# Kernel optimization log

Hardware: AMD Instinct MI355X
Metric: run time of the kernel (lower is better)

The kernel has to match this reference:

```python
import jax, jax.numpy as jnp
import numpy as np
from jax.scipy.special import logsumexp

B, L = 32, 128
NEG = -1e9
SPAN_LAMB = 0.5


def setup_inputs() -> dict:
    key = jax.random.key(0)
    ks = jax.random.split(key, 8)
    span_logits = jax.random.normal(ks[0], (B, L, L, 2), jnp.float32)
    ph = jax.random.normal(ks[1], (B, L, L), jnp.float32)
    pt = jax.random.normal(ks[2], (B, L, L), jnp.float32)
    ph_arc = jax.random.normal(ks[3], (B, L, L), jnp.float32)
    spans_ind = jax.random.randint(ks[4], (B, L, L), 0, 3, jnp.int32)
    ph_ind = jax.random.randint(ks[5], (B, L, L), 0, 2, jnp.int32)
    pt_ind = jax.random.randint(ks[6], (B, L, L), 0, 2, jnp.int32)
    lens = jax.random.randint(ks[7], (B,), L // 2, L + 1, jnp.int32)
    i = jnp.arange(L)
    # maskspan[b,i,j] = valid right-closed span i..j within sentence b; row 0 sums to lens
    maskspan = (i[None, :, None] <= i[None, None, :]) & (i[None, None, :] < lens[:, None, None])
    maskarc = (i[None, :, None] < lens[:, None, None]) & (i[None, None, :] < lens[:, None, None])
    return dict(span_logits=span_logits, ph=ph, pt=pt, ph_arc=ph_arc,
                spans_ind=spans_ind, ph_ind=ph_ind, pt_ind=pt_ind,
                maskspan=maskspan, maskarc=maskarc)


def _inside_logZ(span_logits, lens):
    # CYK inside algorithm over right-closed spans; returns sum_b logZ_b.
    scores = logsumexp(span_logits, axis=-1)  # [B,L,L] span score = lse over labels
    Ln = scores.shape[1]
    ar = jnp.arange(Ln)
    # width-0 base: s[i,i] = scores[i,i]
    s0 = jnp.where(jnp.eye(Ln, dtype=bool)[None], scores, NEG)
    li = ar[:, None] + ar[None, :]        # [L,L]: left child right end i+k
    ri = li + 1                           # right child left end i+k+1
    li_c = jnp.clip(li, 0, Ln - 1)
    ri_c = jnp.clip(ri, 0, Ln - 1)

    def step(s, w):
        j = ar + w
        jc = jnp.clip(j, 0, Ln - 1)
        left = s[:, ar[:, None], li_c]                 # [B,L,L] left[b,i,k]=s[b,i,i+k]
        right = s[:, ri_c, jc[:, None]]                # right[b,i,k]=s[b,i+k+1,i+w]
        comb = jnp.where(ar[None, None, :] < w, left + right, NEG)
        new = scores[:, ar, jc] + logsumexp(comb, axis=-1)  # [B,L]
        valid = (j < Ln)[None, :]
        cur = s[:, ar, jc]
        s = s.at[:, ar, jc].set(jnp.where(valid, new, cur))
        return s, None

    s, _ = jax.lax.scan(step, s0, jnp.arange(1, Ln))
    logZ = jnp.take_along_axis(s[:, 0, :], (lens - 1)[:, None], axis=1)[:, 0]
    return logZ.sum()


def _bce_mean(x, y, m):
    # stable BCEWithLogits, mean over masked elements
    l = jnp.maximum(x, 0.0) - x * y + jnp.log1p(jnp.exp(-jnp.abs(x)))
    return jnp.where(m, l, 0.0).sum() / m.sum().astype(jnp.float32)


def reference(span_logits, ph, pt, ph_arc, spans_ind, ph_ind, pt_ind, maskspan, maskarc):
    lens = maskspan[:, 0].sum(-1)                         # [B]
    spans_b = jnp.where(spans_ind > 0, spans_ind - 1, spans_ind).astype(bool)
    # label marginals = d logZ / d span_logits (matches torch autograd-based cyk)
    marginals = jax.grad(_inside_logZ)(span_logits, lens)  # [B,L,L,2]
    pos_mask = maskspan & spans_b
    neg_mask = maskspan & (~spans_b)
    pos_loss = jnp.log(jnp.where(pos_mask, jnp.maximum(marginals[..., 1], 1e-38), 1.0)).sum()
    neg_loss = jnp.log(jnp.where(neg_mask, jnp.maximum(marginals[..., 0], 1e-38), 1.0)).sum()
    loss_spans = -(pos_loss + neg_loss) / lens.sum().astype(jnp.float32)
    loss_ph = _bce_mean(ph, ph_ind.astype(jnp.float32), maskarc)
    loss_pt = _bce_mean(pt, pt_ind.astype(jnp.float32), maskarc)
    return SPAN_LAMB * loss_spans + (1.0 - SPAN_LAMB) * (loss_ph + loss_pt)
```

## Files before the change

kernel.cpp:

```cpp
#include <hip/hip_runtime.h>
#include <hip/hip_bf16.h>
#include <float.h>

#define NB 32
#define NBCE 32
#define L 128
#define NT 1024
#define R 132
#define PAD 160
#define LOGMIN -87.49823f

__device__ __forceinline__ int mask_mode(const void* p) {
    unsigned int v = ((const unsigned int*)p)[0];
    if (v == 1u) return 1;
    if (v == 0x3F800000u) return 2;
    return 0;
}
__device__ __forceinline__ bool mask_at(const void* p, int mode, int idx) {
    if (mode == 1) return ((const int*)p)[idx] != 0;
    if (mode == 2) return ((const float*)p)[idx] != 0.0f;
    return ((const unsigned char*)p)[idx] != 0;
}

__device__ __forceinline__ float lse2(float a, float b) {
    return fmaxf(a, b) + log1pf(__expf(-fabsf(a - b)));
}

template<int C>
__device__ __forceinline__ float dppf(float x) {
    return __int_as_float(__builtin_amdgcn_mov_dpp(__float_as_int(x), C, 0xF, 0xF, true));
}
__device__ __forceinline__ float bfly8_max(float x) {
    x = fmaxf(x, dppf<0xB1>(x));
    x = fmaxf(x, dppf<0x4E>(x));
    x = fmaxf(x, dppf<0x141>(x));
    return x;
}
__device__ __forceinline__ float bfly8_add(float x) {
    x += dppf<0xB1>(x);
    x += dppf<0x4E>(x);
    x += dppf<0x141>(x);
    return x;
}

template<int NUMAX>
__device__ __forceinline__ void load_pairs(float* buf, int sub, int lo, int hi,
                                           const float* p1, const float* p2, float& mloc) {
    p1 += sub; p2 += sub;
#pragma unroll
    for (int kk = 0; kk < NUMAX; kk += 2) {
        if (kk * 8 >= hi) break;
        const int o0 = kk * 8, o1 = o0 + 8;
        float a0 = p1[o0] + p2[o0];
        float a1 = p1[o1] + p2[o1];
        const int t0 = sub + o0, t1 = sub + o1;
        a0 = (t0 >= lo && t0 < hi) ? a0 : -FLT_MAX;
        a1 = (t1 >= lo && t1 < hi) ? a1 : -FLT_MAX;
        buf[kk] = a0; buf[kk + 1] = a1;
        mloc = fmaxf(mloc, fmaxf(a0, a1));
    }
}
template<int NUMAX>
__device__ __forceinline__ void sum_exp8(const float* buf, int hi, float M, float& s) {
#pragma unroll
    for (int kk = 0; kk < NUMAX; kk += 2) {
        if (kk * 8 >= hi) break;
        s += __expf(buf[kk] - M) + __expf(buf[kk + 1] - M);
    }
}

__global__ __launch_bounds__(NT, 1) void tree_dp_kernel(
    const float* __restrict__ logits,
    const int*   __restrict__ spans_ind,
    const void*  __restrict__ maskspan,
    const float* __restrict__ ph, const float* __restrict__ pt,
    const int* __restrict__ ph_ind, const int* __restrict__ pt_ind,
    const void* __restrict__ maskarc,
    double*      __restrict__ ws)
{
    const int tid = threadIdx.x;

    if (blockIdx.x >= NB) {
        const int mode = mask_mode(maskarc);
        const int tot = NB * L * L;
        double sph = 0.0, spt = 0.0, cnt = 0.0;
        for (int idx = (blockIdx.x - NB) * NT + tid; idx < tot; idx += NBCE * NT) {
            if (mask_at(maskarc, mode, idx)) {
                float x = ph[idx]; float y = (float)ph_ind[idx];
                sph += (double)(fmaxf(x, 0.0f) - x * y + log1pf(__expf(-fabsf(x))));
                x = pt[idx]; y = (float)pt_ind[idx];
                spt += (double)(fmaxf(x, 0.0f) - x * y + log1pf(__expf(-fabsf(x))));
                cnt += 1.0;
            }
        }
        for (int off = 32; off > 0; off >>= 1) {
            sph += __shfl_down(sph, off);
            spt += __shfl_down(spt, off);
            cnt += __shfl_down(cnt, off);
        }
        if ((tid & 63) == 0) {
            atomicAdd(&ws[2], sph); atomicAdd(&ws[3], spt); atomicAdd(&ws[4], cnt);
        }
        return;
    }

    __shared__ float Am[L * R + PAD];
    __shared__ float Gm[L * R + PAD];

    const int b = blockIdx.x;
    const int mbase = b * L * L;
    const int mode = mask_mode(maskspan);

    int pred = (tid < L) && mask_at(maskspan, mode, mbase + tid);
    const int n = __syncthreads_count(pred);

    const float* lg = logits + (size_t)b * L * L * 2;
    const int* si = spans_ind + mbase;

    for (int e = tid; e < L * L; e += NT) {
        int ii = e >> 7, jj = e & (L - 1);
        if (ii <= jj && jj < n) {
            const float* p = lg + (size_t)e * 2;
            float v = lse2(p[0], p[1]);
            Am[ii * R + jj] = v; Am[jj * R + ii] = v;
            Gm[ii * R + jj] = v; Gm[jj * R + ii] = v;
        }
    }
    __syncthreads();

    const int i = tid >> 3;
    const int sub = tid & 7;
    double local = 0.0;
    float buf1[16], buf2[16];

    float ld0 = 0.f, pv = 0.f, scij = 0.f, rjd = 0.f;
    float m_part = -FLT_MAX, s_part = 0.f;
    if (i < n) ld0 = Am[i * R + i];
    if (i < n - 1) scij = Am[i * R + i + 1];

    for (int w = 1; w < n; ++w) {
        const int c = n - w;
        const int j = i + w;
        float r0 = 0.f;
        if (i < c) r0 = Am[j * R + i + 1];
        float nsc = 0.f, nrjd = 0.f, mloc = -FLT_MAX;
        const bool pf = (i < c - 1);
        if (pf) {
            nsc  = Am[i * R + (j + 1)];
            nrjd = Am[(j + 1) * R + (j + 1)];
            load_pairs<16>(buf1, sub, 1, w, &Am[i * R + i], &Am[(j + 1) * R + i + 1], mloc);
        }
        if (i < c) {
            float ta = ld0 + r0;
            float tb = (w >= 2) ? (pv + rjd) : -FLT_MAX;
            float M = fmaxf(fmaxf(m_part, ta), tb);
            float S = s_part * __expf(m_part - M) + __expf(ta - M) + __expf(tb - M);
            float val = scij + M + __logf(S);
            if (sub == 0) { Am[i * R + j] = val; Am[j * R + i] = val; }
            pv = val;
        }
        m_part = -FLT_MAX; s_part = 0.f;
        if (pf) {
            float Mp = bfly8_max(mloc);
            float s = 0.f;
            sum_exp8<16>(buf1, w, Mp, s);
            s_part = bfly8_add(s);
            m_part = Mp;
            scij = nsc; rjd = nrjd;
        }
        __syncthreads();
    }

    const float logZ = Am[n - 1];

    float adI = 0.f, adJ = 0.f, scO = 0.f;
    if (i >= 1 && i < n) adI = Am[(i - 1) * R + (i - 1)];
    if (i == 0) pv = Gm[n - 1];

    m_part = -FLT_MAX; s_part = 0.f;
    {
        const int w1 = n - 2;
        if (i < n - w1) {
            const int j1 = i + w1;
            scO = Gm[i * R + j1];
            if (j1 < n - 1) adJ = Am[(j1 + 1) * R + (j1 + 1)];
            const int nt1 = n - 1 - j1;
            float mloc = -FLT_MAX;
            load_pairs<16>(buf1, sub, 1, nt1, &Gm[i * R + j1 + 1], &Am[(j1 + 1) * R + j1 + 1], mloc);
            load_pairs<16>(buf2, sub, 0, i - 1, &Gm[j1 * R], &Am[(i - 1) * R], mloc);
            float Mp = bfly8_max(mloc);
            float s = 0.f;
            sum_exp8<16>(buf1, nt1, Mp, s);
            sum_exp8<16>(buf2, i - 1, Mp, s);
            s_part = bfly8_add(s);
            m_part = Mp;
        }
    }

    for (int w = n - 2; w >= 0; --w) {
        const int c = n - w;
        const int j = i + w;
        float r0g = 0.f;
        if (i < c && i >= 1) r0g = Gm[j * R + (i - 1)];
        float nsc = 0.f, nadJ = 0.f, mloc = -FLT_MAX;
        const bool pf = (w >= 1) && (i < c + 1);
        int nt1 = 0;
        if (pf) {
            const int j1 = i + w - 1;
            nsc = Gm[i * R + j1];
            if (j1 < n - 1) nadJ = Am[(j1 + 1) * R + (j1 + 1)];
            nt1 = n - 1 - j1;
            load_pairs<16>(buf1, sub, 1, nt1, &Gm[i * R + j1 + 1], &Am[(j1 + 1) * R + j1 + 1], mloc);
            load_pairs<16>(buf2, sub, 0, i - 1, &Gm[j1 * R], &Am[(i - 1) * R], mloc);
        }
        if (i < c) {
            float g1n = (j < n - 1) ? (pv + adJ) : -FLT_MAX;
            float g2n = (i >= 1) ? (r0g + adI) : -FLT_MAX;
            float M = fmaxf(fmaxf(m_part, g1n), g2n);
            float S = s_part * __expf(m_part - M) + __expf(g1n - M) + __expf(g2n - M);
            if (w >= 1) {
                float val = scO + M + __logf(S);
                if (sub == 0) { Gm[i * R + j] = val; Gm[j * R + i] = val; }
                pv = val;
            } else if (sub == 0) {
                float beta_ii = M + __logf(S);
                const float* p = lg + ((size_t)i * L + i) * 2;
                float lc = (si[i * L + i] == 2) ? p[1] : p[0];
                local += (double)fmaxf(beta_ii - logZ + lc, LOGMIN);
            }
        }
        m_part = -FLT_MAX; s_part = 0.f;
        if (pf) {
            float Mp = bfly8_max(mloc);
            float s = 0.f;
            sum_exp8<16>(buf1, nt1, Mp, s);
            sum_exp8<16>(buf2, i - 1, Mp, s);
            s_part = bfly8_add(s);
            m_part = Mp;
            scO = nsc; adJ = nadJ;
        }
        __syncthreads();
    }

    for (int e = tid; e < L * L; e += NT) {
        int ii = e >> 7, jj = e & (L - 1);
        if (ii < jj && jj < n) {
            const float* p = lg + (size_t)e * 2;
            float a = p[0], cc = p[1];
            float sc = lse2(a, cc);
            float lc = (si[e] == 2) ? cc : a;
            float logm = Am[ii * R + jj] + Gm[ii * R + jj] - logZ + lc - 2.0f * sc;
            local += (double)fmaxf(logm, LOGMIN);
        }
    }

    for (int off = 32; off > 0; off >>= 1)
        local += __shfl_down(local, off);
    if ((tid & 63) == 0) atomicAdd(&ws[0], local);
    if (tid == 0) atomicAdd(&ws[1], (double)n);
}

__global__ void finalize_kernel(const double* __restrict__ ws, float* __restrict__ out) {
    double loss_spans = -ws[0] / ws[1];
    double bce = (ws[2] + ws[3]) / ws[4];
    out[0] = (float)(0.5 * loss_spans + 0.5 * bce);
}

extern "C" void kernel_launch(void* const* d_in, const int* in_sizes, int n_in,
                              void* d_out, int out_size, void* d_ws, size_t ws_size,
                              hipStream_t stream) {
    (void)in_sizes; (void)n_in; (void)out_size; (void)ws_size;
    const float* span_logits = (const float*)d_in[0];
    const float* ph          = (const float*)d_in[1];
    const float* pt          = (const float*)d_in[2];
    const int*   spans_ind   = (const int*)d_in[4];
    const int*   ph_ind      = (const int*)d_in[5];
    const int*   pt_ind      = (const int*)d_in[6];
    const void*  maskspan    = d_in[7];
    const void*  maskarc     = d_in[8];
    double* ws = (double*)d_ws;
    float* out = (float*)d_out;

    hipMemsetAsync(d_ws, 0, 5 * sizeof(double), stream);
    hipLaunchKernelGGL(tree_dp_kernel, dim3(NB + NBCE), dim3(NT), 0, stream,
                       span_logits, spans_ind, maskspan,
                       ph, pt, ph_ind, pt_ind, maskarc, ws);
    hipLaunchKernelGGL(finalize_kernel, dim3(1), dim3(1), 0, stream, ws, out);
}
```

Baseline: 343.6 us.

## Pack inside/outside into one square matrix and run two sentences per block

Stores inside scores in the upper triangle and outside scores in the lower triangle of a single shared matrix, so each block holds two sentences and only 16 DP blocks are launched. Each 512-thread half processes one sentence, with every 8-lane group handling two cells per width. The register prefetch pipeline is dropped in favour of a simpler per-cell load, reduce and store. This halves the number of DP blocks and removes the separate outside matrix, but every thread now does two cells serially per step and both halves synchronise to the longer sentence.

```diff
diff --git a/kernel.cpp b/kernel.cpp
--- a/kernel.cpp
+++ b/kernel.cpp
@@ -1,13 +1,13 @@
 #include <hip/hip_runtime.h>
-#include <hip/hip_bf16.h>
 #include <float.h>
 
-#define NB 32
+#define NBATCH 32
+#define NBDP 16
 #define NBCE 32
 #define L 128
 #define NT 1024
 #define R 132
-#define PAD 160
+#define SQ_SIZE (L * R + 8)
 #define LOGMIN -87.49823f
 
 __device__ __forceinline__ int mask_mode(const void* p) {
@@ -30,13 +30,13 @@
 __device__ __forceinline__ float dppf(float x) {
     return __int_as_float(__builtin_amdgcn_mov_dpp(__float_as_int(x), C, 0xF, 0xF, true));
 }
-__device__ __forceinline__ float bfly8_max(float x) {
+__device__ __forceinline__ float bfly_max8(float x) {
     x = fmaxf(x, dppf<0xB1>(x));
     x = fmaxf(x, dppf<0x4E>(x));
     x = fmaxf(x, dppf<0x141>(x));
     return x;
 }
-__device__ __forceinline__ float bfly8_add(float x) {
+__device__ __forceinline__ float bfly_add8(float x) {
     x += dppf<0xB1>(x);
     x += dppf<0x4E>(x);
     x += dppf<0x141>(x);
@@ -44,29 +44,60 @@
 }
 
 template<int NUMAX>
-__device__ __forceinline__ void load_pairs(float* buf, int sub, int lo, int hi,
-                                           const float* p1, const float* p2, float& mloc) {
-    p1 += sub; p2 += sub;
+__device__ __forceinline__ void load_rc(float* v, int sub, int nterm,
+                                        const float* p1, const float* p2, float& mloc) {
+    p1 += sub; p2 += sub * R;
 #pragma unroll
-    for (int kk = 0; kk < NUMAX; kk += 2) {
-        if (kk * 8 >= hi) break;
-        const int o0 = kk * 8, o1 = o0 + 8;
-        float a0 = p1[o0] + p2[o0];
-        float a1 = p1[o1] + p2[o1];
-        const int t0 = sub + o0, t1 = sub + o1;
-        a0 = (t0 >= lo && t0 < hi) ? a0 : -FLT_MAX;
-        a1 = (t1 >= lo && t1 < hi) ? a1 : -FLT_MAX;
-        buf[kk] = a0; buf[kk + 1] = a1;
+    for (int m = 0; m < NUMAX; m += 2) {
+        if (m * 8 >= nterm) break;
+        const int o0 = m * 8, o1 = o0 + 8;
+        float a0 = p1[o0] + p2[o0 * R];
+        float a1 = p1[o1] + p2[o1 * R];
+        a0 = (sub + o0 < nterm) ? a0 : -FLT_MAX;
+        a1 = (sub + o1 < nterm) ? a1 : -FLT_MAX;
+        v[m] = a0; v[m + 1] = a1;
         mloc = fmaxf(mloc, fmaxf(a0, a1));
     }
 }
 template<int NUMAX>
-__device__ __forceinline__ void sum_exp8(const float* buf, int hi, float M, float& s) {
+__device__ __forceinline__ void sum_exp8(const float* v, int nterm, float M, float& s) {
 #pragma unroll
-    for (int kk = 0; kk < NUMAX; kk += 2) {
-        if (kk * 8 >= hi) break;
-        s += __expf(buf[kk] - M) + __expf(buf[kk + 1] - M);
-    }
+    for (int m = 0; m < NUMAX; m += 2) {
+        if (m * 8 >= nterm) break;
+        s += __expf(v[m] - M) + __expf(v[m + 1] - M);
+    }
+}
+
+template<int NU>
+__device__ __forceinline__ void inside_cell(float* SQm, int i, int w, int sub) {
+    const int j = i + w;
+    float v[NU]; float mloc = -FLT_MAX;
+    load_rc<NU>(v, sub, w, &SQm[i * R + i], &SQm[(i + 1) * R + j], mloc);
+    float M = bfly_max8(mloc);
+    float s = 0.0f;
+    sum_exp8<NU>(v, w, M, s);
+    float S = bfly_add8(s);
+    if (sub == 0) SQm[i * R + j] += M + __logf(S);
+}
+
+template<int NU, int NV>
+__device__ __forceinline__ float outside_cell(float* SQm, int i, int j, int n, int sub, bool store) {
+    float v1[NU], v2[NV]; float mloc = -FLT_MAX;
+    const int ntU = n - 1 - j;
+    load_rc<NU>(v1, sub, ntU, &SQm[(j + 1) * R + (j + 1)], &SQm[(j + 1) * R + i], mloc);
+    const float* p2v = &SQm[(i >= 1 ? i - 1 : 0)];
+    load_rc<NV>(v2, sub, i, &SQm[j * R], p2v, mloc);
+    float M = bfly_max8(mloc);
+    float s = 0.0f;
+    sum_exp8<NU>(v1, ntU, M, s);
+    sum_exp8<NV>(v2, i, M, s);
+    float S = bfly_add8(s);
+    float out = 0.0f;
+    if (sub == 0) {
+        out = M + __logf(S);
+        if (store) SQm[j * R + i] += out;
+    }
+    return out;
 }
 
 __global__ __launch_bounds__(NT, 1) void tree_dp_kernel(
@@ -80,11 +111,11 @@
 {
     const int tid = threadIdx.x;
 
-    if (blockIdx.x >= NB) {
+    if (blockIdx.x >= NBDP) {
         const int mode = mask_mode(maskarc);
-        const int tot = NB * L * L;
+        const int tot = NBATCH * L * L;
         double sph = 0.0, spt = 0.0, cnt = 0.0;
-        for (int idx = (blockIdx.x - NB) * NT + tid; idx < tot; idx += NBCE * NT) {
+        for (int idx = (blockIdx.x - NBDP) * NT + tid; idx < tot; idx += NBCE * NT) {
             if (mask_at(maskarc, mode, idx)) {
                 float x = ph[idx]; float y = (float)ph_ind[idx];
                 sph += (double)(fmaxf(x, 0.0f) - x * y + log1pf(__expf(-fabsf(x))));
@@ -104,152 +135,81 @@
         return;
     }
 
-    __shared__ float Am[L * R + PAD];
-    __shared__ float Gm[L * R + PAD];
-
-    const int b = blockIdx.x;
-    const int mbase = b * L * L;
+    __shared__ __align__(16) float SQ[2][SQ_SIZE];
+
+    const int half = tid >> 9;
+    const int t = tid & 511;
+    const int bA = blockIdx.x * 2, bB = bA + 1;
+    const int bmy = half ? bB : bA;
+
     const int mode = mask_mode(maskspan);
-
-    int pred = (tid < L) && mask_at(maskspan, mode, mbase + tid);
-    const int n = __syncthreads_count(pred);
-
-    const float* lg = logits + (size_t)b * L * L * 2;
-    const int* si = spans_ind + mbase;
-
-    for (int e = tid; e < L * L; e += NT) {
+    int predA = (tid < L) && mask_at(maskspan, mode, bA * L * L + tid);
+    const int nA = __syncthreads_count(predA);
+    int predB = (tid < L) && mask_at(maskspan, mode, bB * L * L + tid);
+    const int nB = __syncthreads_count(predB);
+    const int n = half ? nB : nA;
+    const int nmax = max(nA, nB);
+
+    float* SQm = SQ[half];
+    const float* lg = logits + (size_t)bmy * L * L * 2;
+    const int* si = spans_ind + (size_t)bmy * L * L;
+
+    for (int e = t; e < L * L; e += 512) {
         int ii = e >> 7, jj = e & (L - 1);
         if (ii <= jj && jj < n) {
             const float* p = lg + (size_t)e * 2;
             float v = lse2(p[0], p[1]);
-            Am[ii * R + jj] = v; Am[jj * R + ii] = v;
-            Gm[ii * R + jj] = v; Gm[jj * R + ii] = v;
+            SQm[ii * R + jj] = v;
+            if (ii < jj) SQm[jj * R + ii] = v;
         }
     }
     __syncthreads();
 
-    const int i = tid >> 3;
-    const int sub = tid & 7;
+    const int sg = t >> 3, sub = t & 7;
+
+    for (int w = 1; w < nmax; ++w) {
+        if (w < n) {
+            const int c = n - w;
+            if (sg < c) inside_cell<16>(SQm, sg, w, sub);
+            if (sg + 64 < c) inside_cell<8>(SQm, sg + 64, w, sub);
+        }
+        __syncthreads();
+    }
+
+    const float logZ = SQm[n - 1];
+
+    for (int w = nmax - 2; w >= 1; --w) {
+        if (w <= n - 2) {
+            const int c = n - w;
+            if (sg < c) outside_cell<16, 8>(SQm, sg, sg + w, n, sub, true);
+            if (sg + 64 < c) outside_cell<8, 16>(SQm, sg + 64, sg + 64 + w, n, sub, true);
+        }
+        __syncthreads();
+    }
+
     double local = 0.0;
-    float buf1[16], buf2[16];
-
-    float ld0 = 0.f, pv = 0.f, scij = 0.f, rjd = 0.f;
-    float m_part = -FLT_MAX, s_part = 0.f;
-    if (i < n) ld0 = Am[i * R + i];
-    if (i < n - 1) scij = Am[i * R + i + 1];
-
-    for (int w = 1; w < n; ++w) {
-        const int c = n - w;
-        const int j = i + w;
-        float r0 = 0.f;
-        if (i < c) r0 = Am[j * R + i + 1];
-        float nsc = 0.f, nrjd = 0.f, mloc = -FLT_MAX;
-        const bool pf = (i < c - 1);
-        if (pf) {
-            nsc  = Am[i * R + (j + 1)];
-            nrjd = Am[(j + 1) * R + (j + 1)];
-            load_pairs<16>(buf1, sub, 1, w, &Am[i * R + i], &Am[(j + 1) * R + i + 1], mloc);
-        }
-        if (i < c) {
-            float ta = ld0 + r0;
-            float tb = (w >= 2) ? (pv + rjd) : -FLT_MAX;
-            float M = fmaxf(fmaxf(m_part, ta), tb);
-            float S = s_part * __expf(m_part - M) + __expf(ta - M) + __expf(tb - M);
-            float val = scij + M + __logf(S);
-            if (sub == 0) { Am[i * R + j] = val; Am[j * R + i] = val; }
-            pv = val;
-        }
-        m_part = -FLT_MAX; s_part = 0.f;
-        if (pf) {
-            float Mp = bfly8_max(mloc);
-            float s = 0.f;
-            sum_exp8<16>(buf1, w, Mp, s);
-            s_part = bfly8_add(s);
-            m_part = Mp;
-            scij = nsc; rjd = nrjd;
-        }
-        __syncthreads();
-    }
-
-    const float logZ = Am[n - 1];
-
-    float adI = 0.f, adJ = 0.f, scO = 0.f;
-    if (i >= 1 && i < n) adI = Am[(i - 1) * R + (i - 1)];
-    if (i == 0) pv = Gm[n - 1];
-
-    m_part = -FLT_MAX; s_part = 0.f;
-    {
-        const int w1 = n - 2;
-        if (i < n - w1) {
-            const int j1 = i + w1;
-            scO = Gm[i * R + j1];
-            if (j1 < n - 1) adJ = Am[(j1 + 1) * R + (j1 + 1)];
-            const int nt1 = n - 1 - j1;
-            float mloc = -FLT_MAX;
-            load_pairs<16>(buf1, sub, 1, nt1, &Gm[i * R + j1 + 1], &Am[(j1 + 1) * R + j1 + 1], mloc);
-            load_pairs<16>(buf2, sub, 0, i - 1, &Gm[j1 * R], &Am[(i - 1) * R], mloc);
-            float Mp = bfly8_max(mloc);
-            float s = 0.f;
-            sum_exp8<16>(buf1, nt1, Mp, s);
-            sum_exp8<16>(buf2, i - 1, Mp, s);
-            s_part = bfly8_add(s);
-            m_part = Mp;
-        }
-    }
-
-    for (int w = n - 2; w >= 0; --w) {
-        const int c = n - w;
-        const int j = i + w;
-        float r0g = 0.f;
-        if (i < c && i >= 1) r0g = Gm[j * R + (i - 1)];
-        float nsc = 0.f, nadJ = 0.f, mloc = -FLT_MAX;
-        const bool pf = (w >= 1) && (i < c + 1);
-        int nt1 = 0;
-        if (pf) {
-            const int j1 = i + w - 1;
-            nsc = Gm[i * R + j1];
-            if (j1 < n - 1) nadJ = Am[(j1 + 1) * R + (j1 + 1)];
-            nt1 = n - 1 - j1;
-            load_pairs<16>(buf1, sub, 1, nt1, &Gm[i * R + j1 + 1], &Am[(j1 + 1) * R + j1 + 1], mloc);
-            load_pairs<16>(buf2, sub, 0, i - 1, &Gm[j1 * R], &Am[(i - 1) * R], mloc);
-        }
-        if (i < c) {
-            float g1n = (j < n - 1) ? (pv + adJ) : -FLT_MAX;
-            float g2n = (i >= 1) ? (r0g + adI) : -FLT_MAX;
-            float M = fmaxf(fmaxf(m_part, g1n), g2n);
-            float S = s_part * __expf(m_part - M) + __expf(g1n - M) + __expf(g2n - M);
-            if (w >= 1) {
-                float val = scO + M + __logf(S);
-                if (sub == 0) { Gm[i * R + j] = val; Gm[j * R + i] = val; }
-                pv = val;
-            } else if (sub == 0) {
-                float beta_ii = M + __logf(S);
+#pragma unroll
+    for (int pass = 0; pass < 2; ++pass) {
+        const int i = sg + pass * 64;
+        if (i < n) {
+            float beta = (pass == 0) ? outside_cell<16, 8>(SQm, i, i, n, sub, false)
+                                     : outside_cell<8, 16>(SQm, i, i, n, sub, false);
+            if (sub == 0) {
                 const float* p = lg + ((size_t)i * L + i) * 2;
                 float lc = (si[i * L + i] == 2) ? p[1] : p[0];
-                local += (double)fmaxf(beta_ii - logZ + lc, LOGMIN);
+                local += (double)fmaxf(beta - logZ + lc, LOGMIN);
             }
         }
-        m_part = -FLT_MAX; s_part = 0.f;
-        if (pf) {
-            float Mp = bfly8_max(mloc);
-            float s = 0.f;
-            sum_exp8<16>(buf1, nt1, Mp, s);
-            sum_exp8<16>(buf2, i - 1, Mp, s);
-            s_part = bfly8_add(s);
-            m_part = Mp;
-            scO = nsc; adJ = nadJ;
-        }
-        __syncthreads();
-    }
-
-    for (int e = tid; e < L * L; e += NT) {
+    }
+
+    for (int e = t; e < L * L; e += 512) {
         int ii = e >> 7, jj = e & (L - 1);
         if (ii < jj && jj < n) {
             const float* p = lg + (size_t)e * 2;
             float a = p[0], cc = p[1];
             float sc = lse2(a, cc);
             float lc = (si[e] == 2) ? cc : a;
-            float logm = Am[ii * R + jj] + Gm[ii * R + jj] - logZ + lc - 2.0f * sc;
+            float logm = SQm[ii * R + jj] + SQm[jj * R + ii] - logZ + lc - 2.0f * sc;
             local += (double)fmaxf(logm, LOGMIN);
         }
     }
@@ -257,7 +217,7 @@
     for (int off = 32; off > 0; off >>= 1)
         local += __shfl_down(local, off);
     if ((tid & 63) == 0) atomicAdd(&ws[0], local);
-    if (tid == 0) atomicAdd(&ws[1], (double)n);
+    if (t == 0) atomicAdd(&ws[1], (double)n);
 }
 
 __global__ void finalize_kernel(const double* __restrict__ ws, float* __restrict__ out) {
@@ -282,7 +242,7 @@
     float* out = (float*)d_out;
 
     hipMemsetAsync(d_ws, 0, 5 * sizeof(double), stream);
-    hipLaunchKernelGGL(tree_dp_kernel, dim3(NB + NBCE), dim3(NT), 0, stream,
+    hipLaunchKernelGGL(tree_dp_kernel, dim3(NBDP + NBCE), dim3(NT), 0, stream,
                        span_logits, spans_ind, maskspan,
                        ph, pt, ph_ind, pt_ind, maskarc, ws);
     hipLaunchKernelGGL(finalize_kernel, dim3(1), dim3(1), 0, stream, ws, out);
```

Measured after the change: 408.8 us. 1.19x slower.
